# Kernel optimization log

Hardware: AMD Instinct MI355X
Metric: run time of the kernel (lower is better)

Reference implementation:

```python
import jax, jax.numpy as jnp
import numpy as np

S = 8192          # sequence length
E = 1024          # embedding_dim
H = 2048          # hidden_dim
V = 50257         # vocab_size
T = 50            # tagset_size


def setup_inputs() -> dict:
    key = jax.random.key(0)
    ks = jax.random.split(key, 5)
    scale = 0.02
    return {
        "sentence": jax.random.randint(ks[0], (S,), 0, V),
        "emb": jax.random.normal(ks[1], (V, E), jnp.float32) * scale,
        "W_ih": jax.random.normal(ks[2], (H, E), jnp.float32) * scale,
        "W_hh": jax.random.normal(ks[3], (H, H), jnp.float32) * scale,
        "b_ih": jnp.zeros((H,), jnp.float32),
        "b_hh": jnp.zeros((H,), jnp.float32),
        "W_out": jax.random.normal(ks[4], (T, H), jnp.float32) * scale,
        "b_out": jnp.zeros((T,), jnp.float32),
        "h0": jnp.zeros((H,), jnp.float32),
    }


def reference(sentence, emb, W_ih, W_hh, b_ih, b_hh, W_out, b_out, h0):
    # Embedding lookup: [S, E]
    x = emb[sentence]
    # Precompute input contribution for all timesteps (parallel GEMM): [S, H]
    xi = x @ W_ih.T + b_ih + b_hh

    # Elman recurrence: h_t = tanh(W_ih x_t + b_ih + W_hh h_{t-1} + b_hh)
    def step(h, xi_t):
        h_new = jnp.tanh(xi_t + W_hh @ h)
        return h_new, h_new

    _, rnn_out = jax.lax.scan(step, h0, xi)  # rnn_out: [S, H]

    # Linear head + log_softmax over tags
    tag_space = rnn_out @ W_out.T + b_out    # [S, T]
    return jax.nn.log_softmax(tag_space, axis=-1)
```

## Files before the change

kernel.cpp:

```cpp
#include <hip/hip_runtime.h>
#include <hip/hip_bf16.h>

#define S_LEN 8192
#define E_DIM 1024
#define H_DIM 2048
#define T_TAGS 50
#define NWG 256
#define RPW (H_DIM / NWG)

typedef short short8 __attribute__((ext_vector_type(8)));
typedef float floatx4 __attribute__((ext_vector_type(4)));
typedef _Float16 half8 __attribute__((ext_vector_type(8)));
typedef _Float16 half2v __attribute__((ext_vector_type(2)));
typedef unsigned int uint4a __attribute__((ext_vector_type(4)));

__device__ __forceinline__ unsigned short f2bf(float f) {
    unsigned u = __builtin_bit_cast(unsigned, f);
    unsigned r = (u + 0x7fffu + ((u >> 16) & 1u)) >> 16;
    return (unsigned short)r;
}

__device__ __forceinline__ float dot8(half8 a, half8 b, float acc) {
#if __has_builtin(__builtin_amdgcn_fdot2)
    union U { half8 v; half2v p[4]; };
    U ua; ua.v = a; U ub; ub.v = b;
    acc = __builtin_amdgcn_fdot2(ua.p[0], ub.p[0], acc, false);
    acc = __builtin_amdgcn_fdot2(ua.p[1], ub.p[1], acc, false);
    acc = __builtin_amdgcn_fdot2(ua.p[2], ub.p[2], acc, false);
    acc = __builtin_amdgcn_fdot2(ua.p[3], ub.p[3], acc, false);
#else
    #pragma unroll
    for (int i = 0; i < 8; ++i) acc += (float)a[i] * (float)b[i];
#endif
    return acc;
}

__device__ __forceinline__ void load2x16_coherent(const uint4a* p, uint4a& a, uint4a& b) {
    asm volatile(
        "global_load_dwordx4 %0, %2, off sc0 sc1\n\t"
        "global_load_dwordx4 %1, %3, off sc0 sc1\n\t"
        "s_waitcnt vmcnt(0)"
        : "=&v"(a), "=&v"(b)
        : "v"(p), "v"(p + 1)
        : "memory");
}

__global__ __launch_bounds__(256) void cast_kernel(
        const float* __restrict__ whh, const float* __restrict__ wih,
        const float* __restrict__ wout,
        _Float16* __restrict__ whh_h, unsigned short* __restrict__ wih_b,
        _Float16* __restrict__ wout_h) {
    const int nWhh = H_DIM * H_DIM;
    const int nWih = H_DIM * E_DIM;
    const int nWout = 64 * H_DIM;
    long long i = (long long)blockIdx.x * 256 + threadIdx.x;
    if (i < nWhh) { whh_h[i] = (_Float16)whh[i]; return; }
    i -= nWhh;
    if (i < nWih) { wih_b[i] = f2bf(wih[i]); return; }
    i -= nWih;
    if (i < nWout) {
        int r = (int)(i >> 11), c = (int)(i & 2047);
        wout_h[i] = (r < T_TAGS) ? (_Float16)wout[r * H_DIM + c] : (_Float16)0.f;
    }
}

__global__ __launch_bounds__(256) void embed_kernel(
        const int* __restrict__ sent, const float* __restrict__ emb,
        unsigned short* __restrict__ Xb) {
    size_t i = (size_t)blockIdx.x * 256 + threadIdx.x;
    size_t s = i >> 10, e = i & 1023;
    Xb[i] = f2bf(emb[(size_t)sent[s] * E_DIM + e]);
}

__global__ __launch_bounds__(256) void xi_gemm(
        const unsigned short* __restrict__ Xb, const unsigned short* __restrict__ Wb,
        const float* __restrict__ bih, const float* __restrict__ bhh,
        float* __restrict__ xi) {
    int lane = threadIdx.x & 63;
    int w = threadIdx.x >> 6;
    int m0 = blockIdx.y * 64 + w * 16;
    int n0 = blockIdx.x * 16;
    int mi = m0 + (lane & 15);
    int ni = n0 + (lane & 15);
    int q8 = (lane >> 4) * 8;
    const short8* arow = (const short8*)(Xb + (size_t)mi * E_DIM + q8);
    const short8* brow = (const short8*)(Wb + (size_t)ni * E_DIM + q8);
    floatx4 acc = {0.f, 0.f, 0.f, 0.f};
    #pragma unroll 4
    for (int k = 0; k < E_DIM / 32; ++k) {
        short8 a = arow[k * 4];
        short8 b = brow[k * 4];
        acc = __builtin_amdgcn_mfma_f32_16x16x32_bf16(a, b, acc, 0, 0, 0);
    }
    float bias = bih[ni] + bhh[ni];
    int rbase = (lane >> 4) * 4;
    #pragma unroll
    for (int i = 0; i < 4; ++i) {
        xi[(size_t)(m0 + rbase + i) * H_DIM + ni] = acc[i] + bias;
    }
}

__global__ __launch_bounds__(256) void init_hpk(
        const float* __restrict__ h0, unsigned* __restrict__ hpk) {
    int i = blockIdx.x * 256 + threadIdx.x;
    if (i < H_DIM) {
        unsigned short hb = __builtin_bit_cast(unsigned short, (_Float16)h0[i]);
        hpk[i] = (unsigned)hb;
        hpk[H_DIM + i] = 0xFFFF0000u;
    }
}

__global__ __launch_bounds__(256, 1) void rnn_seq(
        const _Float16* __restrict__ Whh, const float* __restrict__ xi,
        unsigned* __restrict__ hpk, _Float16* __restrict__ rnn) {
    __shared__ __align__(16) _Float16 wlds[RPW][H_DIM];
    __shared__ __align__(16) _Float16 hlds[2][H_DIM];
    __shared__ float xilds[2][RPW];
    const int tid = threadIdx.x;
    const int wg = blockIdx.x;
    const int rowbase = wg * RPW;

    {
        const uint4* gsrc = (const uint4*)(Whh + (size_t)rowbase * H_DIM);
        uint4* ldst = (uint4*)&wlds[0][0];
        for (int i = tid; i < RPW * H_DIM / 8; i += 256) ldst[i] = gsrc[i];
    }
    if (tid < RPW) xilds[0][tid] = xi[rowbase + tid];
    __syncthreads();

    const int r = tid >> 5;
    const int j = tid & 31;

    for (int t = 0; t < S_LEN; ++t) {
        float xnext = 0.f;
        if (tid < RPW && t + 1 < S_LEN) xnext = xi[(size_t)(t + 1) * H_DIM + rowbase + tid];

        const uint4a* p = (const uint4a*)(hpk + (size_t)(t & 1) * H_DIM) + tid * 2;
        const unsigned tg = (unsigned)t;
        uint4a a, b;
        bool ok;
        do {
            load2x16_coherent(p, a, b);
            ok = ((a.x >> 16) == tg) & ((a.y >> 16) == tg) &
                 ((a.z >> 16) == tg) & ((a.w >> 16) == tg) &
                 ((b.x >> 16) == tg) & ((b.y >> 16) == tg) &
                 ((b.z >> 16) == tg) & ((b.w >> 16) == tg);
        } while (!ok);

        uint4a hp;
        hp.x = (a.x & 0xffffu) | (a.y << 16);
        hp.y = (a.z & 0xffffu) | (a.w << 16);
        hp.z = (b.x & 0xffffu) | (b.y << 16);
        hp.w = (b.z & 0xffffu) | (b.w << 16);
        *(uint4a*)&hlds[t & 1][tid * 8] = hp;
        if (tid < RPW) xilds[(t + 1) & 1][tid] = xnext;
        __syncthreads();

        float acc = 0.f;
        const _Float16* wp = &wlds[r][j * 8];
        const _Float16* hpt = &hlds[t & 1][j * 8];
        #pragma unroll
        for (int c = 0; c < 8; ++c) {
            half8 wv = *(const half8*)(wp + c * 256);
            half8 hv = *(const half8*)(hpt + c * 256);
            acc = dot8(wv, hv, acc);
        }

        acc += __shfl_xor(acc, 1);  acc += __shfl_xor(acc, 2);
        acc += __shfl_xor(acc, 4);  acc += __shfl_xor(acc, 8);
        acc += __shfl_xor(acc, 16);

        if (j == 0) {
            float hv = tanhf(xilds[t & 1][r] + acc);
            _Float16 hf = (_Float16)hv;
            unsigned pk = ((unsigned)(t + 1) << 16)
                        | (unsigned)__builtin_bit_cast(unsigned short, hf);
            __hip_atomic_store(&hpk[(size_t)((t + 1) & 1) * H_DIM + rowbase + r], pk,
                               __ATOMIC_RELAXED, __HIP_MEMORY_SCOPE_AGENT);
            rnn[(size_t)t * H_DIM + rowbase + r] = hf;
        }
    }
}

__global__ __launch_bounds__(256) void head_kernel(
        const _Float16* __restrict__ rnn, const _Float16* __restrict__ Wout,
        const float* __restrict__ bout, float* __restrict__ out) {
    __shared__ __align__(16) _Float16 h8[8][H_DIM];
    __shared__ __align__(16) _Float16 wr[H_DIM];
    __shared__ float tl[8][T_TAGS];
    int tid = threadIdx.x;
    size_t sbase = (size_t)blockIdx.x * 8;
    {
        const uint4* src = (const uint4*)(rnn + sbase * H_DIM);
        uint4* dst = (uint4*)&h8[0][0];
        for (int i = tid; i < 8 * H_DIM / 8; i += 256) dst[i] = src[i];
    }
    __syncthreads();
    int sl = ((tid >> 6) << 1) | ((tid >> 5) & 1);
    int l32 = tid & 31;
    for (int t = 0; t < T_TAGS; ++t) {
        ((uint4*)wr)[tid] = ((const uint4*)(Wout + t * H_DIM))[tid];
        __syncthreads();
        float acc = 0.f;
        const _Float16* hp = &h8[sl][l32 * 64];
        const _Float16* wp = &wr[l32 * 64];
        #pragma unroll
        for (int c = 0; c < 8; ++c)
            acc = dot8(*(const half8*)(hp + c * 8), *(const half8*)(wp + c * 8), acc);
        acc += __shfl_xor(acc, 1);  acc += __shfl_xor(acc, 2);
        acc += __shfl_xor(acc, 4);  acc += __shfl_xor(acc, 8);
        acc += __shfl_xor(acc, 16);
        if (l32 == 0) tl[sl][t] = acc + bout[t];
        __syncthreads();
    }
    if (tid < 8) {
        float m = -1e30f;
        for (int t = 0; t < T_TAGS; ++t) m = fmaxf(m, tl[tid][t]);
        float sum = 0.f;
        for (int t = 0; t < T_TAGS; ++t) sum += expf(tl[tid][t] - m);
        float lse = m + logf(sum);
        for (int t = 0; t < T_TAGS; ++t) out[(sbase + tid) * T_TAGS + t] = tl[tid][t] - lse;
    }
}

extern "C" void kernel_launch(void* const* d_in, const int* in_sizes, int n_in,
                              void* d_out, int out_size, void* d_ws, size_t ws_size,
                              hipStream_t stream) {
    const int*   sent = (const int*)  d_in[0];
    const float* emb  = (const float*)d_in[1];
    const float* wih  = (const float*)d_in[2];
    const float* whh  = (const float*)d_in[3];
    const float* bih  = (const float*)d_in[4];
    const float* bhh  = (const float*)d_in[5];
    const float* wout = (const float*)d_in[6];
    const float* bout = (const float*)d_in[7];
    const float* h0   = (const float*)d_in[8];

    char* ws = (char*)d_ws;
    _Float16*       whh_h  = (_Float16*)      (ws + 0);
    unsigned short* wih_b  = (unsigned short*)(ws + 8388608);
    _Float16*       wout_h = (_Float16*)      (ws + 12582912);
    unsigned short* X_b    = (unsigned short*)(ws + 12845056);
    unsigned*       hpk    = (unsigned*)      (ws + 29605888);
    float*          xi     = (float*)         (ws + 29622272);
    _Float16*       rnn    = (_Float16*)      (ws + 96731136);

    {
        const int total = H_DIM * H_DIM + H_DIM * E_DIM + 64 * H_DIM;
        cast_kernel<<<(total + 255) / 256, 256, 0, stream>>>(
            whh, wih, wout, whh_h, wih_b, wout_h);
    }
    embed_kernel<<<(S_LEN * E_DIM) / 256, 256, 0, stream>>>(sent, emb, X_b);
    xi_gemm<<<dim3(H_DIM / 16, S_LEN / 64), 256, 0, stream>>>(X_b, wih_b, bih, bhh, xi);
    init_hpk<<<H_DIM / 256, 256, 0, stream>>>(h0, hpk);
    rnn_seq<<<NWG, 256, 0, stream>>>(whh_h, xi, hpk, rnn);
    head_kernel<<<S_LEN / 8, 256, 0, stream>>>(rnn, wout_h, bout, (float*)d_out);
}
```

Measured before the change: 27.40 ms.

## Keep recurrent weights in registers, retry only stale halves, use fast tanh

Each thread now loads its 64 fp16 W_hh weights into registers once, so the per-step reads of those weights from LDS go away. The spin-wait on the packed hidden state now re-polls only the 16-byte half that is still stale, and sleeps briefly after the second failed round. tanhf is replaced by an exp-based formula on a clamped input, which shortens the serial critical path at a small accuracy cost. Holding the weights adds VGPR pressure, and the sleep may add latency to each step.

Measured after the change: 27.67 ms. Within noise of the previous version (+1.0%).

```diff
diff --git a/kernel.cpp b/kernel.cpp
--- a/kernel.cpp
+++ b/kernel.cpp
@@ -33,16 +33,6 @@
     for (int i = 0; i < 8; ++i) acc += (float)a[i] * (float)b[i];
 #endif
     return acc;
-}
-
-__device__ __forceinline__ void load2x16_coherent(const uint4a* p, uint4a& a, uint4a& b) {
-    asm volatile(
-        "global_load_dwordx4 %0, %2, off sc0 sc1\n\t"
-        "global_load_dwordx4 %1, %3, off sc0 sc1\n\t"
-        "s_waitcnt vmcnt(0)"
-        : "=&v"(a), "=&v"(b)
-        : "v"(p), "v"(p + 1)
-        : "memory");
 }
 
 __global__ __launch_bounds__(256) void cast_kernel(
@@ -113,39 +103,47 @@
 __global__ __launch_bounds__(256, 1) void rnn_seq(
         const _Float16* __restrict__ Whh, const float* __restrict__ xi,
         unsigned* __restrict__ hpk, _Float16* __restrict__ rnn) {
-    __shared__ __align__(16) _Float16 wlds[RPW][H_DIM];
     __shared__ __align__(16) _Float16 hlds[2][H_DIM];
     __shared__ float xilds[2][RPW];
     const int tid = threadIdx.x;
     const int wg = blockIdx.x;
     const int rowbase = wg * RPW;
-
+    const int r = tid >> 5;
+    const int j = tid & 31;
+
+    half8 wreg[8];
     {
-        const uint4* gsrc = (const uint4*)(Whh + (size_t)rowbase * H_DIM);
-        uint4* ldst = (uint4*)&wlds[0][0];
-        for (int i = tid; i < RPW * H_DIM / 8; i += 256) ldst[i] = gsrc[i];
+        const half8* wrow = (const half8*)(Whh + (size_t)(rowbase + r) * H_DIM);
+        #pragma unroll
+        for (int c = 0; c < 8; ++c) wreg[c] = wrow[j + c * 32];
     }
     if (tid < RPW) xilds[0][tid] = xi[rowbase + tid];
     __syncthreads();
-
-    const int r = tid >> 5;
-    const int j = tid & 31;
 
     for (int t = 0; t < S_LEN; ++t) {
         float xnext = 0.f;
         if (tid < RPW && t + 1 < S_LEN) xnext = xi[(size_t)(t + 1) * H_DIM + rowbase + tid];
 
-        const uint4a* p = (const uint4a*)(hpk + (size_t)(t & 1) * H_DIM) + tid * 2;
+        const uint4a* p0 = (const uint4a*)(hpk + (size_t)(t & 1) * H_DIM) + tid * 2;
         const unsigned tg = (unsigned)t;
-        uint4a a, b;
-        bool ok;
-        do {
-            load2x16_coherent(p, a, b);
-            ok = ((a.x >> 16) == tg) & ((a.y >> 16) == tg) &
-                 ((a.z >> 16) == tg) & ((a.w >> 16) == tg) &
-                 ((b.x >> 16) == tg) & ((b.y >> 16) == tg) &
-                 ((b.z >> 16) == tg) & ((b.w >> 16) == tg);
-        } while (!ok);
+        uint4a a = {}, b = {};
+        bool got0 = false, got1 = false;
+        int round = 0;
+        for (;;) {
+            if (!got0)
+                asm volatile("global_load_dwordx4 %0, %1, off sc0 sc1"
+                             : "=v"(a) : "v"(p0) : "memory");
+            if (!got1)
+                asm volatile("global_load_dwordx4 %0, %1, off sc0 sc1"
+                             : "=v"(b) : "v"(p0 + 1) : "memory");
+            asm volatile("s_waitcnt vmcnt(0)" ::: "memory");
+            got0 = got0 | (((a.x >> 16) == tg) & ((a.y >> 16) == tg) &
+                           ((a.z >> 16) == tg) & ((a.w >> 16) == tg));
+            got1 = got1 | (((b.x >> 16) == tg) & ((b.y >> 16) == tg) &
+                           ((b.z >> 16) == tg) & ((b.w >> 16) == tg));
+            if (got0 && got1) break;
+            if (++round > 1) __builtin_amdgcn_s_sleep(1);
+        }
 
         uint4a hp;
         hp.x = (a.x & 0xffffu) | (a.y << 16);
@@ -157,13 +155,11 @@
         __syncthreads();
 
         float acc = 0.f;
-        const _Float16* wp = &wlds[r][j * 8];
         const _Float16* hpt = &hlds[t & 1][j * 8];
         #pragma unroll
         for (int c = 0; c < 8; ++c) {
-            half8 wv = *(const half8*)(wp + c * 256);
             half8 hv = *(const half8*)(hpt + c * 256);
-            acc = dot8(wv, hv, acc);
+            acc = dot8(wreg[c], hv, acc);
         }
 
         acc += __shfl_xor(acc, 1);  acc += __shfl_xor(acc, 2);
@@ -171,7 +167,10 @@
         acc += __shfl_xor(acc, 16);
 
         if (j == 0) {
-            float hv = tanhf(xilds[t & 1][r] + acc);
+            float x = xilds[t & 1][r] + acc;
+            float xc = fminf(fmaxf(x, -9.f), 9.f);
+            float e = __expf(2.f * xc);
+            float hv = (e - 1.f) / (e + 1.f);
             _Float16 hf = (_Float16)hv;
             unsigned pk = ((unsigned)(t + 1) << 16)
                         | (unsigned)__builtin_bit_cast(unsigned short, hf);
```
